# Kernel optimization log

Hardware: AMD Instinct MI355X
Metric: run time of the kernel (lower is better)

Reference implementation:

```python
import jax, jax.numpy as jnp
import numpy as np

NINP = 1024
NHID = 1024
BATCH = 16384
EPS = 1e-5


def _ln(x, g, b):
    mu = jnp.mean(x, axis=-1, keepdims=True)
    var = jnp.mean(jnp.square(x - mu), axis=-1, keepdims=True)
    return (x - mu) * jax.lax.rsqrt(var + EPS) * g + b


def setup_inputs() -> dict:
    key = jax.random.key(0)
    ks = jax.random.split(key, 12)
    s_i = 1.0 / np.sqrt(NINP)
    s_h = 1.0 / np.sqrt(NHID)
    return {
        "inp": jax.random.normal(ks[0], (BATCH, NINP), jnp.float32),
        "hidden": jax.random.normal(ks[1], (BATCH, NHID), jnp.float32),
        "W_i2gate": jax.random.uniform(ks[2], (3 * NHID, NINP), jnp.float32, -s_i, s_i),
        "b_i2gate": jnp.zeros((3 * NHID,), jnp.float32),
        "W_h2gate": jax.random.uniform(ks[3], (3 * NHID, NHID), jnp.float32, -s_h, s_h),
        "b_h2gate": jnp.zeros((3 * NHID,), jnp.float32),
        "W_i2i": jax.random.uniform(ks[4], (NHID, NINP), jnp.float32, -s_i, s_i),
        "b_i2i": jnp.zeros((NHID,), jnp.float32),
        "W_i2h": jax.random.uniform(ks[5], (NHID, NINP), jnp.float32, -s_i, s_i),
        "b_i2h": jnp.zeros((NHID,), jnp.float32),
        "W_h2h": jax.random.uniform(ks[6], (NHID, NHID), jnp.float32, -s_h, s_h),
        "b_h2h": jnp.zeros((NHID,), jnp.float32),
        "g_ig": jnp.ones((3 * NHID,), jnp.float32),
        "be_ig": jnp.zeros((3 * NHID,), jnp.float32),
        "g_hg": jnp.ones((3 * NHID,), jnp.float32),
        "be_hg": jnp.zeros((3 * NHID,), jnp.float32),
        "g_ii": jnp.ones((NHID,), jnp.float32),
        "be_ii": jnp.zeros((NHID,), jnp.float32),
        "g_ih": jnp.ones((NHID,), jnp.float32),
        "be_ih": jnp.zeros((NHID,), jnp.float32),
        "g_hh": jnp.ones((NHID,), jnp.float32),
        "be_hh": jnp.zeros((NHID,), jnp.float32),
    }


def reference(inp, hidden, W_i2gate, b_i2gate, W_h2gate, b_h2gate,
              W_i2i, b_i2i, W_i2h, b_i2h, W_h2h, b_h2h,
              g_ig, be_ig, g_hg, be_hg, g_ii, be_ii,
              g_ih, be_ih, g_hh, be_hh):
    gate = jax.nn.sigmoid(
        _ln(inp @ W_i2gate.T + b_i2gate, g_ig, be_ig)
        + _ln(hidden @ W_h2gate.T + b_h2gate, g_hg, be_hg))
    r, z, g = jnp.split(gate, 3, axis=-1)
    Hx = _ln(inp @ W_i2i.T + b_i2i, g_ii, be_ii)
    xh = _ln(inp @ W_i2h.T + b_i2h, g_ih, be_ih)
    hh = _ln(hidden @ W_h2h.T + b_h2h, g_hh, be_hh)
    hidden_m = jnp.tanh((1.0 - r) * xh + r * hh)
    return ((1.0 - z) * hidden + z * hidden_m) * (1.0 - g) + g * Hx
```

## Files before the change

kernel.cpp:

```cpp
#include <hip/hip_runtime.h>

typedef __bf16 bf16_t;
typedef bf16_t bf16x8 __attribute__((ext_vector_type(8)));
typedef bf16_t bf16x4 __attribute__((ext_vector_type(4)));
typedef float f32x4 __attribute__((ext_vector_type(4)));

#define BATCH 16384
#define KDIM  1024
#define NCOLS 9216

#define BMg 256
#define BNg 256
#define BKg 64
#define NTg (KDIM / BKg)
#define NBN (NCOLS / BNg)

__global__ __launch_bounds__(256)
void cast_all(const float* __restrict__ Wig, const float* __restrict__ Wii,
              const float* __restrict__ Wih, const float* __restrict__ Whg,
              const float* __restrict__ Whh,
              const float* __restrict__ big, const float* __restrict__ bii,
              const float* __restrict__ bih, const float* __restrict__ bhg,
              const float* __restrict__ bhh,
              const float* __restrict__ inp, const float* __restrict__ hid,
              bf16_t* __restrict__ Wcat, float* __restrict__ bcat,
              bf16_t* __restrict__ inpb, bf16_t* __restrict__ hidb,
              int nact_units, int ntot)
{
  int u = blockIdx.x * 256 + threadIdx.x;
  if (u >= ntot) return;

  if (u < 2359296) {
    const float* src; int off;
    if      (u < 786432)  { src = Wig; off = u; }
    else if (u < 1048576) { src = Wii; off = u - 786432; }
    else if (u < 1310720) { src = Wih; off = u - 1048576; }
    else if (u < 2097152) { src = Whg; off = u - 1310720; }
    else                  { src = Whh; off = u - 2097152; }
    float4 v = reinterpret_cast<const float4*>(src)[off];
    bf16x4 o;
    o[0] = (bf16_t)v.x; o[1] = (bf16_t)v.y; o[2] = (bf16_t)v.z; o[3] = (bf16_t)v.w;
    reinterpret_cast<bf16x4*>(Wcat)[u] = o;
  } else if (u < 2361600) {
    int bu = u - 2359296;
    int i = bu * 4;
    const float* src; int off;
    if      (i < 3072) { src = big; off = i; }
    else if (i < 4096) { src = bii; off = i - 3072; }
    else if (i < 5120) { src = bih; off = i - 4096; }
    else if (i < 8192) { src = bhg; off = i - 5120; }
    else               { src = bhh; off = i - 8192; }
    reinterpret_cast<float4*>(bcat)[bu] = *reinterpret_cast<const float4*>(src + off);
  } else {
    int au = u - 2361600;
    const float* src; bf16_t* dst; int off;
    if (au < nact_units) { src = inp; dst = inpb; off = au; }
    else                 { src = hid; dst = hidb; off = au - nact_units; }
    float4 v = reinterpret_cast<const float4*>(src)[off];
    bf16x4 o;
    o[0] = (bf16_t)v.x; o[1] = (bf16_t)v.y; o[2] = (bf16_t)v.z; o[3] = (bf16_t)v.w;
    reinterpret_cast<bf16x4*>(dst)[off] = o;
  }
}

__global__ __launch_bounds__(256)
void cast_acts(const float* __restrict__ inp, const float* __restrict__ hid,
               bf16_t* __restrict__ inpb, bf16_t* __restrict__ hidb, int n4) {
  int i = blockIdx.x * 256 + threadIdx.x;
  if (i >= 2 * n4) return;
  const float* src = (i < n4) ? inp : hid;
  bf16_t* dst = (i < n4) ? inpb : hidb;
  int off = (i < n4) ? i : i - n4;
  float4 v = reinterpret_cast<const float4*>(src)[off];
  bf16x4 o;
  o[0] = (bf16_t)v.x; o[1] = (bf16_t)v.y; o[2] = (bf16_t)v.z; o[3] = (bf16_t)v.w;
  reinterpret_cast<bf16x4*>(dst)[off] = o;
}

__global__ __launch_bounds__(512, 2)
void gemm_preln(const bf16_t* __restrict__ inpb, const bf16_t* __restrict__ hidb,
                const bf16_t* __restrict__ Wcat, const float* __restrict__ bcat,
                bf16_t* __restrict__ preLN, int nbm)
{
  __shared__ alignas(16) char lds_raw[131072];

  const int tid  = threadIdx.x;
  const int wid  = tid >> 6;
  const int lane = tid & 63;
  const int fr   = lane & 15;
  const int kg   = lane >> 4;
  const int wr   = wid >> 2;
  const int wc   = wid & 3;

  const int nwg = nbm * NBN;
  int orig = blockIdx.x;
  int q_ = nwg >> 3, r_ = nwg & 7, xcd = orig & 7, idx = orig >> 3;
  int wg = (xcd < r_ ? xcd * (q_ + 1) : r_ * (q_ + 1) + (xcd - r_) * q_) + idx;
  const int bm = wg / NBN, bn = wg % NBN;
  const int row0 = bm * BMg, col0 = bn * BNg;
  const bf16_t* __restrict__ act = (col0 < 5120) ? inpb : hidb;
  const bf16_t* __restrict__ wgt = Wcat + (size_t)col0 * KDIM;

  const int r_st  = tid >> 2;
  const int k8_st = (tid & 3) ^ ((r_st >> 1) & 3);
  const bf16_t* pA = act + (size_t)(row0 + r_st) * KDIM + k8_st * 8;
  const bf16_t* pB = wgt + (size_t)r_st * KDIM + k8_st * 8;

  auto stage_half = [&](int mat, int h, int T) {
    const bf16_t* s = (mat ? pB : pA) + ((size_t)h * 128) * KDIM + T * BKg;
    char* d = lds_raw + ((T & 1) << 16) + (mat << 15) + (h << 14) + (wid << 10);
    __builtin_amdgcn_global_load_lds(
        (const __attribute__((address_space(1))) unsigned int*)s,
        (__attribute__((address_space(3))) unsigned int*)d, 16, 0, 0);
    __builtin_amdgcn_global_load_lds(
        (const __attribute__((address_space(1))) unsigned int*)(s + 32),
        (__attribute__((address_space(3))) unsigned int*)(d + 8192), 16, 0, 0);
  };

  int offA[4][2], offB[2][2];
  #pragma unroll
  for (int m = 0; m < 4; ++m)
    #pragma unroll
    for (int ks = 0; ks < 2; ++ks) {
      const int rowA = wr * 64 + m * 16 + fr;
      offA[m][ks] = ks * 8192 + rowA * 64 + ((kg ^ ((rowA >> 1) & 3)) << 4);
    }
  #pragma unroll
  for (int n = 0; n < 2; ++n)
    #pragma unroll
    for (int ks = 0; ks < 2; ++ks) {
      const int rowB = wc * 32 + n * 16 + fr;
      offB[n][ks] = ks * 8192 + rowB * 64 + ((kg ^ ((rowB >> 1) & 3)) << 4);
    }

  f32x4 acc[2][4][2][2] = {};

  stage_half(0, 0, 0); stage_half(1, 0, 0);
  stage_half(0, 1, 0); stage_half(1, 1, 0);
  stage_half(0, 0, 1); stage_half(1, 0, 1);
  asm volatile("s_waitcnt vmcnt(4)" ::: "memory");
  __builtin_amdgcn_s_barrier();

  for (int T = 0; T < NTg; ++T) {
    const int bufo = (T & 1) << 16;
    bf16x8 a[4][2], b0[2][2], b1[2][2];

    #pragma unroll
    for (int m = 0; m < 4; ++m)
      #pragma unroll
      for (int ks = 0; ks < 2; ++ks)
        a[m][ks] = *(const bf16x8*)(lds_raw + bufo + offA[m][ks]);
    #pragma unroll
    for (int n = 0; n < 2; ++n)
      #pragma unroll
      for (int ks = 0; ks < 2; ++ks)
        b0[n][ks] = *(const bf16x8*)(lds_raw + bufo + 32768 + offB[n][ks]);
    if (T + 1 < NTg) stage_half(0, 1, T + 1);
    __builtin_amdgcn_s_barrier();
    asm volatile("s_waitcnt lgkmcnt(0)" ::: "memory");
    __builtin_amdgcn_sched_barrier(0);
    __builtin_amdgcn_s_setprio(1);
    #pragma unroll
    for (int m = 0; m < 4; ++m)
      #pragma unroll
      for (int n = 0; n < 2; ++n)
        #pragma unroll
        for (int ks = 0; ks < 2; ++ks)
          acc[0][m][0][n] = __builtin_amdgcn_mfma_f32_16x16x32_bf16(a[m][ks], b0[n][ks], acc[0][m][0][n], 0, 0, 0);
    __builtin_amdgcn_s_setprio(0);
    __builtin_amdgcn_s_barrier();

    #pragma unroll
    for (int n = 0; n < 2; ++n)
      #pragma unroll
      for (int ks = 0; ks < 2; ++ks)
        b1[n][ks] = *(const bf16x8*)(lds_raw + bufo + 32768 + 16384 + offB[n][ks]);
    if (T + 1 < NTg) stage_half(1, 1, T + 1);
    __builtin_amdgcn_s_barrier();
    asm volatile("s_waitcnt lgkmcnt(0)" ::: "memory");
    __builtin_amdgcn_sched_barrier(0);
    __builtin_amdgcn_s_setprio(1);
    #pragma unroll
    for (int m = 0; m < 4; ++m)
      #pragma unroll
      for (int n = 0; n < 2; ++n)
        #pragma unroll
        for (int ks = 0; ks < 2; ++ks)
          acc[0][m][1][n] = __builtin_amdgcn_mfma_f32_16x16x32_bf16(a[m][ks], b1[n][ks], acc[0][m][1][n], 0, 0, 0);
    __builtin_amdgcn_s_setprio(0);
    __builtin_amdgcn_s_barrier();

    #pragma unroll
    for (int m = 0; m < 4; ++m)
      #pragma unroll
      for (int ks = 0; ks < 2; ++ks)
        a[m][ks] = *(const bf16x8*)(lds_raw + bufo + 16384 + offA[m][ks]);
    if (T + 2 < NTg) stage_half(0, 0, T + 2);
    __builtin_amdgcn_s_barrier();
    asm volatile("s_waitcnt lgkmcnt(0)" ::: "memory");
    __builtin_amdgcn_sched_barrier(0);
    __builtin_amdgcn_s_setprio(1);
    #pragma unroll
    for (int m = 0; m < 4; ++m)
      #pragma unroll
      for (int n = 0; n < 2; ++n)
        #pragma unroll
        for (int ks = 0; ks < 2; ++ks)
          acc[1][m][1][n] = __builtin_amdgcn_mfma_f32_16x16x32_bf16(a[m][ks], b1[n][ks], acc[1][m][1][n], 0, 0, 0);
    __builtin_amdgcn_s_setprio(0);
    __builtin_amdgcn_s_barrier();

    if (T + 2 < NTg) stage_half(1, 0, T + 2);
    __builtin_amdgcn_s_barrier();
    __builtin_amdgcn_s_setprio(1);
    #pragma unroll
    for (int m = 0; m < 4; ++m)
      #pragma unroll
      for (int n = 0; n < 2; ++n)
        #pragma unroll
        for (int ks = 0; ks < 2; ++ks)
          acc[1][m][0][n] = __builtin_amdgcn_mfma_f32_16x16x32_bf16(a[m][ks], b0[n][ks], acc[1][m][0][n], 0, 0, 0);
    __builtin_amdgcn_s_setprio(0);

    if (T < NTg - 2) {
      asm volatile("s_waitcnt vmcnt(4)" ::: "memory");
      __builtin_amdgcn_s_barrier();
    } else if (T == NTg - 2) {
      asm volatile("s_waitcnt vmcnt(0)" ::: "memory");
      __builtin_amdgcn_s_barrier();
    }
  }

  #pragma unroll
  for (int qn_ = 0; qn_ < 2; ++qn_)
    #pragma unroll
    for (int n = 0; n < 2; ++n) {
      const int col = col0 + qn_ * 128 + wc * 32 + n * 16 + fr;
      const float bias = bcat[col];
      #pragma unroll
      for (int qm_ = 0; qm_ < 2; ++qm_)
        #pragma unroll
        for (int m = 0; m < 4; ++m) {
          const int rbase = row0 + qm_ * 128 + wr * 64 + m * 16 + kg * 4;
          #pragma unroll
          for (int j = 0; j < 4; ++j)
            preLN[(size_t)(rbase + j) * NCOLS + col] = (bf16_t)(acc[qm_][m][qn_][n][j] + bias);
        }
    }
}

__global__ __launch_bounds__(256)
void ln_combine(const bf16_t* __restrict__ preLN, const float* __restrict__ hidden,
                const float* __restrict__ g_ig, const float* __restrict__ be_ig,
                const float* __restrict__ g_hg, const float* __restrict__ be_hg,
                const float* __restrict__ g_ii, const float* __restrict__ be_ii,
                const float* __restrict__ g_ih, const float* __restrict__ be_ih,
                const float* __restrict__ g_hh, const float* __restrict__ be_hh,
                float* __restrict__ out)
{
  __shared__ alignas(16) bf16_t rowbuf[NCOLS];
  __shared__ float wsum[4][10];
  __shared__ float stats[10];
  const int tid = threadIdx.x;
  const int wv  = tid >> 6;
  const int ln  = tid & 63;
  const size_t row = blockIdx.x;
  const bf16_t* __restrict__ src = preLN + row * NCOLS;

  float s1[5] = {0.f, 0.f, 0.f, 0.f, 0.f};
  float s2[5] = {0.f, 0.f, 0.f, 0.f, 0.f};
  #pragma unroll
  for (int j = 0; j < 9; ++j) {
    const int idx = j * 1024 + tid * 4;
    bf16x4 v = *(const bf16x4*)&src[idx];
    *(bf16x4*)&rowbuf[idx] = v;
    const int sg = (j < 3) ? 0 : (j == 3) ? 1 : (j == 4) ? 2 : (j < 8) ? 3 : 4;
    const float f0 = (float)v[0], f1 = (float)v[1], f2 = (float)v[2], f3 = (float)v[3];
    s1[sg] += f0 + f1 + f2 + f3;
    s2[sg] += f0 * f0 + f1 * f1 + f2 * f2 + f3 * f3;
  }
  #pragma unroll
  for (int s = 0; s < 5; ++s)
    #pragma unroll
    for (int off = 32; off; off >>= 1) {
      s1[s] += __shfl_xor(s1[s], off);
      s2[s] += __shfl_xor(s2[s], off);
    }
  if (ln == 0) {
    #pragma unroll
    for (int s = 0; s < 5; ++s) { wsum[wv][s] = s1[s]; wsum[wv][5 + s] = s2[s]; }
  }
  __syncthreads();
  if (tid < 5) {
    const float n = (tid == 0 || tid == 3) ? 3072.f : 1024.f;
    float t1 = wsum[0][tid] + wsum[1][tid] + wsum[2][tid] + wsum[3][tid];
    float t2 = wsum[0][5 + tid] + wsum[1][5 + tid] + wsum[2][5 + tid] + wsum[3][5 + tid];
    float mu = t1 / n;
    float var = t2 / n - mu * mu;
    stats[tid] = mu;
    stats[5 + tid] = rsqrtf(var + 1e-5f);
  }
  __syncthreads();

  const float mu0 = stats[0], r0 = stats[5];
  const float mu1 = stats[1], r1 = stats[6];
  const float mu2 = stats[2], r2 = stats[7];
  const float mu3 = stats[3], r3 = stats[8];
  const float mu4 = stats[4], r4 = stats[9];
  const float* __restrict__ hrow = hidden + row * 1024;

  const int c = tid * 4;
  bf16x4 v_igr = *(const bf16x4*)&rowbuf[c];
  bf16x4 v_igz = *(const bf16x4*)&rowbuf[c + 1024];
  bf16x4 v_igg = *(const bf16x4*)&rowbuf[c + 2048];
  bf16x4 v_ii  = *(const bf16x4*)&rowbuf[c + 3072];
  bf16x4 v_ih  = *(const bf16x4*)&rowbuf[c + 4096];
  bf16x4 v_hgr = *(const bf16x4*)&rowbuf[c + 5120];
  bf16x4 v_hgz = *(const bf16x4*)&rowbuf[c + 6144];
  bf16x4 v_hgg = *(const bf16x4*)&rowbuf[c + 7168];
  bf16x4 v_hh  = *(const bf16x4*)&rowbuf[c + 8192];

  f32x4 Gr  = *(const f32x4*)&g_ig[c];        f32x4 Br  = *(const f32x4*)&be_ig[c];
  f32x4 Gz  = *(const f32x4*)&g_ig[c + 1024]; f32x4 Bz  = *(const f32x4*)&be_ig[c + 1024];
  f32x4 Gg  = *(const f32x4*)&g_ig[c + 2048]; f32x4 Bg  = *(const f32x4*)&be_ig[c + 2048];
  f32x4 Hr  = *(const f32x4*)&g_hg[c];        f32x4 Cr  = *(const f32x4*)&be_hg[c];
  f32x4 Hz  = *(const f32x4*)&g_hg[c + 1024]; f32x4 Cz  = *(const f32x4*)&be_hg[c + 1024];
  f32x4 Hg  = *(const f32x4*)&g_hg[c + 2048]; f32x4 Cg  = *(const f32x4*)&be_hg[c + 2048];
  f32x4 Gii = *(const f32x4*)&g_ii[c];        f32x4 Bii = *(const f32x4*)&be_ii[c];
  f32x4 Gih = *(const f32x4*)&g_ih[c];        f32x4 Bih = *(const f32x4*)&be_ih[c];
  f32x4 Ghh = *(const f32x4*)&g_hh[c];        f32x4 Bhh = *(const f32x4*)&be_hh[c];
  f32x4 hv  = *(const f32x4*)&hrow[c];

  f32x4 o;
  #pragma unroll
  for (int i = 0; i < 4; ++i) {
    float pr = ((float)v_igr[i] - mu0) * r0 * Gr[i] + Br[i]
             + ((float)v_hgr[i] - mu3) * r3 * Hr[i] + Cr[i];
    float pz = ((float)v_igz[i] - mu0) * r0 * Gz[i] + Bz[i]
             + ((float)v_hgz[i] - mu3) * r3 * Hz[i] + Cz[i];
    float pg = ((float)v_igg[i] - mu0) * r0 * Gg[i] + Bg[i]
             + ((float)v_hgg[i] - mu3) * r3 * Hg[i] + Cg[i];

    float rr = 1.f / (1.f + __expf(-pr));
    float zz = 1.f / (1.f + __expf(-pz));
    float gg = 1.f / (1.f + __expf(-pg));

    float Hx = ((float)v_ii[i] - mu1) * r1 * Gii[i] + Bii[i];
    float xh = ((float)v_ih[i] - mu2) * r2 * Gih[i] + Bih[i];
    float hh = ((float)v_hh[i] - mu4) * r4 * Ghh[i] + Bhh[i];

    float pre = (1.f - rr) * xh + rr * hh;
    float hm  = 1.f - 2.f / (1.f + __expf(2.f * pre));
    o[i] = ((1.f - zz) * hv[i] + zz * hm) * (1.f - gg) + gg * Hx;
  }
  *(f32x4*)&out[row * 1024 + c] = o;
}

extern "C" void kernel_launch(void* const* d_in, const int* in_sizes, int n_in,
                              void* d_out, int out_size, void* d_ws, size_t ws_size,
                              hipStream_t stream) {
  const float* inp      = (const float*)d_in[0];
  const float* hidden   = (const float*)d_in[1];
  const float* W_i2gate = (const float*)d_in[2];
  const float* b_i2gate = (const float*)d_in[3];
  const float* W_h2gate = (const float*)d_in[4];
  const float* b_h2gate = (const float*)d_in[5];
  const float* W_i2i    = (const float*)d_in[6];
  const float* b_i2i    = (const float*)d_in[7];
  const float* W_i2h    = (const float*)d_in[8];
  const float* b_i2h    = (const float*)d_in[9];
  const float* W_h2h    = (const float*)d_in[10];
  const float* b_h2h    = (const float*)d_in[11];
  const float* g_ig  = (const float*)d_in[12];
  const float* be_ig = (const float*)d_in[13];
  const float* g_hg  = (const float*)d_in[14];
  const float* be_hg = (const float*)d_in[15];
  const float* g_ii  = (const float*)d_in[16];
  const float* be_ii = (const float*)d_in[17];
  const float* g_ih  = (const float*)d_in[18];
  const float* be_ih = (const float*)d_in[19];
  const float* g_hh  = (const float*)d_in[20];
  const float* be_hh = (const float*)d_in[21];
  float* out = (float*)d_out;

  const size_t WCAT_B  = (size_t)NCOLS * KDIM * 2;
  const size_t BCAT_B  = (size_t)NCOLS * 4;
  const size_t FIXED_B = WCAT_B + BCAT_B;
  const size_t PER_ROW = 2048 + 2048 + 18432;

  if (ws_size < FIXED_B + PER_ROW * 256) return;

  char* ws = (char*)d_ws;
  bf16_t* Wcat = (bf16_t*)ws;
  float*  bcat = (float*)(ws + WCAT_B);
  char*   dyn  = ws + FIXED_B;

  size_t max_rows = (ws_size - FIXED_B) / PER_ROW;
  int chunk = (int)((max_rows / 256) * 256);
  if (chunk > BATCH) chunk = BATCH;

  bf16_t* inpb  = (bf16_t*)dyn;
  bf16_t* hidb  = (bf16_t*)(dyn + (size_t)chunk * 2048);
  bf16_t* preLN = (bf16_t*)(dyn + (size_t)chunk * 4096);

  if (chunk == BATCH) {
    const int nact = BATCH * KDIM / 4;
    const int ntot = 2361600 + 2 * nact;
    cast_all<<<(ntot + 255) / 256, 256, 0, stream>>>(
        W_i2gate, W_i2i, W_i2h, W_h2gate, W_h2h,
        b_i2gate, b_i2i, b_i2h, b_h2gate, b_h2h,
        inp, hidden, Wcat, bcat, inpb, hidb, nact, ntot);

    int nbm = BATCH / BMg;
    gemm_preln<<<nbm * NBN, 512, 0, stream>>>(inpb, hidb, Wcat, bcat, preLN, nbm);

    ln_combine<<<BATCH, 256, 0, stream>>>(preLN, hidden,
                                          g_ig, be_ig, g_hg, be_hg,
                                          g_ii, be_ii, g_ih, be_ih, g_hh, be_hh,
                                          out);
  } else {
    const int ntot_w = 2361600;
    cast_all<<<(ntot_w + 255) / 256, 256, 0, stream>>>(
        W_i2gate, W_i2i, W_i2h, W_h2gate, W_h2h,
        b_i2gate, b_i2i, b_i2h, b_h2gate, b_h2h,
        nullptr, nullptr, Wcat, bcat, nullptr, nullptr, 0, ntot_w);

    for (int r0 = 0; r0 < BATCH; r0 += chunk) {
      int cr = BATCH - r0;
      if (cr > chunk) cr = chunk;
      int n4 = cr * KDIM / 4;
      cast_acts<<<(2 * n4 + 255) / 256, 256, 0, stream>>>(
          inp + (size_t)r0 * KDIM, hidden + (size_t)r0 * KDIM, inpb, hidb, n4);

      int nbm = cr / BMg;
      gemm_preln<<<nbm * NBN, 512, 0, stream>>>(inpb, hidb, Wcat, bcat, preLN, nbm);

      ln_combine<<<cr, 256, 0, stream>>>(preLN, hidden + (size_t)r0 * KDIM,
                                         g_ig, be_ig, g_hg, be_hg,
                                         g_ii, be_ii, g_ih, be_ih, g_hh, be_hh,
                                         out + (size_t)r0 * KDIM);
    }
  }
}
```

Measured before the change: 499.7 us.

## Switch GEMM to 32x32x16 MFMA and process multiple rows per LN block

The GEMM inner loops move from 16x16x32 bf16 MFMA tiles to 32x32x16 tiles, which changes the LDS fragment offsets, the accumulator layout and the epilogue row mapping. This cuts the number of MFMA issues and LDS reads per tile. Separately, the LayerNorm/combine kernel now handles 8 rows per block, loading gamma/beta once per block and prefetching the next row's preLN values while reducing the current row. The cost is more complex accumulator indexing, and each LN block runs longer in exchange for less per-row setup.

```diff
diff --git a/kernel.cpp b/kernel.cpp
--- a/kernel.cpp
+++ b/kernel.cpp
@@ -4,6 +4,7 @@
 typedef bf16_t bf16x8 __attribute__((ext_vector_type(8)));
 typedef bf16_t bf16x4 __attribute__((ext_vector_type(4)));
 typedef float f32x4 __attribute__((ext_vector_type(4)));
+typedef float f32x16 __attribute__((ext_vector_type(16)));
 
 #define BATCH 16384
 #define KDIM  1024
@@ -14,6 +15,7 @@
 #define BKg 64
 #define NTg (KDIM / BKg)
 #define NBN (NCOLS / BNg)
+#define LNROWS 8
 
 __global__ __launch_bounds__(256)
 void cast_all(const float* __restrict__ Wig, const float* __restrict__ Wii,
@@ -87,8 +89,8 @@
   const int tid  = threadIdx.x;
   const int wid  = tid >> 6;
   const int lane = tid & 63;
-  const int fr   = lane & 15;
-  const int kg   = lane >> 4;
+  const int l31  = lane & 31;
+  const int lk   = lane >> 5;
   const int wr   = wid >> 2;
   const int wc   = wid & 3;
 
@@ -117,23 +119,23 @@
         (__attribute__((address_space(3))) unsigned int*)(d + 8192), 16, 0, 0);
   };
 
-  int offA[4][2], offB[2][2];
+  int offA[2][4], offB[4];
   #pragma unroll
-  for (int m = 0; m < 4; ++m)
-    #pragma unroll
-    for (int ks = 0; ks < 2; ++ks) {
-      const int rowA = wr * 64 + m * 16 + fr;
-      offA[m][ks] = ks * 8192 + rowA * 64 + ((kg ^ ((rowA >> 1) & 3)) << 4);
+  for (int t = 0; t < 2; ++t)
+    #pragma unroll
+    for (int ks = 0; ks < 4; ++ks) {
+      const int rowA = wr * 64 + t * 32 + l31;
+      const int k8 = (ks & 1) * 2 + lk;
+      offA[t][ks] = (ks >> 1) * 8192 + rowA * 64 + ((k8 ^ ((rowA >> 1) & 3)) << 4);
     }
   #pragma unroll
-  for (int n = 0; n < 2; ++n)
-    #pragma unroll
-    for (int ks = 0; ks < 2; ++ks) {
-      const int rowB = wc * 32 + n * 16 + fr;
-      offB[n][ks] = ks * 8192 + rowB * 64 + ((kg ^ ((rowB >> 1) & 3)) << 4);
-    }
-
-  f32x4 acc[2][4][2][2] = {};
+  for (int ks = 0; ks < 4; ++ks) {
+    const int colB = wc * 32 + l31;
+    const int k8 = (ks & 1) * 2 + lk;
+    offB[ks] = (ks >> 1) * 8192 + colB * 64 + ((k8 ^ ((colB >> 1) & 3)) << 4);
+  }
+
+  f32x16 acc[2][2][2] = {};
 
   stage_half(0, 0, 0); stage_half(1, 0, 0);
   stage_half(0, 1, 0); stage_half(1, 1, 0);
@@ -143,70 +145,60 @@
 
   for (int T = 0; T < NTg; ++T) {
     const int bufo = (T & 1) << 16;
-    bf16x8 a[4][2], b0[2][2], b1[2][2];
-
-    #pragma unroll
-    for (int m = 0; m < 4; ++m)
-      #pragma unroll
-      for (int ks = 0; ks < 2; ++ks)
-        a[m][ks] = *(const bf16x8*)(lds_raw + bufo + offA[m][ks]);
-    #pragma unroll
-    for (int n = 0; n < 2; ++n)
-      #pragma unroll
-      for (int ks = 0; ks < 2; ++ks)
-        b0[n][ks] = *(const bf16x8*)(lds_raw + bufo + 32768 + offB[n][ks]);
+    bf16x8 a[2][4], b0[4], b1[4];
+
+    #pragma unroll
+    for (int t = 0; t < 2; ++t)
+      #pragma unroll
+      for (int ks = 0; ks < 4; ++ks)
+        a[t][ks] = *(const bf16x8*)(lds_raw + bufo + offA[t][ks]);
+    #pragma unroll
+    for (int ks = 0; ks < 4; ++ks)
+      b0[ks] = *(const bf16x8*)(lds_raw + bufo + 32768 + offB[ks]);
     if (T + 1 < NTg) stage_half(0, 1, T + 1);
     __builtin_amdgcn_s_barrier();
     asm volatile("s_waitcnt lgkmcnt(0)" ::: "memory");
     __builtin_amdgcn_sched_barrier(0);
     __builtin_amdgcn_s_setprio(1);
     #pragma unroll
-    for (int m = 0; m < 4; ++m)
-      #pragma unroll
-      for (int n = 0; n < 2; ++n)
-        #pragma unroll
-        for (int ks = 0; ks < 2; ++ks)
-          acc[0][m][0][n] = __builtin_amdgcn_mfma_f32_16x16x32_bf16(a[m][ks], b0[n][ks], acc[0][m][0][n], 0, 0, 0);
+    for (int t = 0; t < 2; ++t)
+      #pragma unroll
+      for (int ks = 0; ks < 4; ++ks)
+        acc[0][t][0] = __builtin_amdgcn_mfma_f32_32x32x16_bf16(a[t][ks], b0[ks], acc[0][t][0], 0, 0, 0);
     __builtin_amdgcn_s_setprio(0);
     __builtin_amdgcn_s_barrier();
 
     #pragma unroll
-    for (int n = 0; n < 2; ++n)
-      #pragma unroll
-      for (int ks = 0; ks < 2; ++ks)
-        b1[n][ks] = *(const bf16x8*)(lds_raw + bufo + 32768 + 16384 + offB[n][ks]);
+    for (int ks = 0; ks < 4; ++ks)
+      b1[ks] = *(const bf16x8*)(lds_raw + bufo + 32768 + 16384 + offB[ks]);
     if (T + 1 < NTg) stage_half(1, 1, T + 1);
     __builtin_amdgcn_s_barrier();
     asm volatile("s_waitcnt lgkmcnt(0)" ::: "memory");
     __builtin_amdgcn_sched_barrier(0);
     __builtin_amdgcn_s_setprio(1);
     #pragma unroll
-    for (int m = 0; m < 4; ++m)
-      #pragma unroll
-      for (int n = 0; n < 2; ++n)
-        #pragma unroll
-        for (int ks = 0; ks < 2; ++ks)
-          acc[0][m][1][n] = __builtin_amdgcn_mfma_f32_16x16x32_bf16(a[m][ks], b1[n][ks], acc[0][m][1][n], 0, 0, 0);
+    for (int t = 0; t < 2; ++t)
+      #pragma unroll
+      for (int ks = 0; ks < 4; ++ks)
+        acc[0][t][1] = __builtin_amdgcn_mfma_f32_32x32x16_bf16(a[t][ks], b1[ks], acc[0][t][1], 0, 0, 0);
     __builtin_amdgcn_s_setprio(0);
     __builtin_amdgcn_s_barrier();
 
     #pragma unroll
-    for (int m = 0; m < 4; ++m)
-      #pragma unroll
-      for (int ks = 0; ks < 2; ++ks)
-        a[m][ks] = *(const bf16x8*)(lds_raw + bufo + 16384 + offA[m][ks]);
+    for (int t = 0; t < 2; ++t)
+      #pragma unroll
+      for (int ks = 0; ks < 4; ++ks)
+        a[t][ks] = *(const bf16x8*)(lds_raw + bufo + 16384 + offA[t][ks]);
     if (T + 2 < NTg) stage_half(0, 0, T + 2);
     __builtin_amdgcn_s_barrier();
     asm volatile("s_waitcnt lgkmcnt(0)" ::: "memory");
     __builtin_amdgcn_sched_barrier(0);
     __builtin_amdgcn_s_setprio(1);
     #pragma unroll
-    for (int m = 0; m < 4; ++m)
-      #pragma unroll
-      for (int n = 0; n < 2; ++n)
-        #pragma unroll
-        for (int ks = 0; ks < 2; ++ks)
-          acc[1][m][1][n] = __builtin_amdgcn_mfma_f32_16x16x32_bf16(a[m][ks], b1[n][ks], acc[1][m][1][n], 0, 0, 0);
+    for (int t = 0; t < 2; ++t)
+      #pragma unroll
+      for (int ks = 0; ks < 4; ++ks)
+        acc[1][t][1] = __builtin_amdgcn_mfma_f32_32x32x16_bf16(a[t][ks], b1[ks], acc[1][t][1], 0, 0, 0);
     __builtin_amdgcn_s_setprio(0);
     __builtin_amdgcn_s_barrier();
 
@@ -214,12 +206,10 @@
     __builtin_amdgcn_s_barrier();
     __builtin_amdgcn_s_setprio(1);
     #pragma unroll
-    for (int m = 0; m < 4; ++m)
-      #pragma unroll
-      for (int n = 0; n < 2; ++n)
-        #pragma unroll
-        for (int ks = 0; ks < 2; ++ks)
-          acc[1][m][0][n] = __builtin_amdgcn_mfma_f32_16x16x32_bf16(a[m][ks], b0[n][ks], acc[1][m][0][n], 0, 0, 0);
+    for (int t = 0; t < 2; ++t)
+      #pragma unroll
+      for (int ks = 0; ks < 4; ++ks)
+        acc[1][t][0] = __builtin_amdgcn_mfma_f32_32x32x16_bf16(a[t][ks], b0[ks], acc[1][t][0], 0, 0, 0);
     __builtin_amdgcn_s_setprio(0);
 
     if (T < NTg - 2) {
@@ -232,21 +222,21 @@
   }
 
   #pragma unroll
-  for (int qn_ = 0; qn_ < 2; ++qn_)
-    #pragma unroll
-    for (int n = 0; n < 2; ++n) {
-      const int col = col0 + qn_ * 128 + wc * 32 + n * 16 + fr;
-      const float bias = bcat[col];
-      #pragma unroll
-      for (int qm_ = 0; qm_ < 2; ++qm_)
+  for (int qn_ = 0; qn_ < 2; ++qn_) {
+    const int col = col0 + qn_ * 128 + wc * 32 + l31;
+    const float bias = bcat[col];
+    #pragma unroll
+    for (int qm_ = 0; qm_ < 2; ++qm_)
+      #pragma unroll
+      for (int t = 0; t < 2; ++t) {
+        const int rbase = row0 + qm_ * 128 + wr * 64 + t * 32 + 4 * lk;
         #pragma unroll
-        for (int m = 0; m < 4; ++m) {
-          const int rbase = row0 + qm_ * 128 + wr * 64 + m * 16 + kg * 4;
-          #pragma unroll
-          for (int j = 0; j < 4; ++j)
-            preLN[(size_t)(rbase + j) * NCOLS + col] = (bf16_t)(acc[qm_][m][qn_][n][j] + bias);
+        for (int reg = 0; reg < 16; ++reg) {
+          const int rr = rbase + (reg & 3) + 8 * (reg >> 2);
+          preLN[(size_t)rr * NCOLS + col] = (bf16_t)(acc[qm_][t][qn_][reg] + bias);
         }
-    }
+      }
+  }
 }
 
 __global__ __launch_bounds__(256)
@@ -264,96 +254,116 @@
   const int tid = threadIdx.x;
   const int wv  = tid >> 6;
   const int ln  = tid & 63;
-  const size_t row = blockIdx.x;
-  const bf16_t* __restrict__ src = preLN + row * NCOLS;
-
-  float s1[5] = {0.f, 0.f, 0.f, 0.f, 0.f};
-  float s2[5] = {0.f, 0.f, 0.f, 0.f, 0.f};
-  #pragma unroll
-  for (int j = 0; j < 9; ++j) {
-    const int idx = j * 1024 + tid * 4;
-    bf16x4 v = *(const bf16x4*)&src[idx];
-    *(bf16x4*)&rowbuf[idx] = v;
-    const int sg = (j < 3) ? 0 : (j == 3) ? 1 : (j == 4) ? 2 : (j < 8) ? 3 : 4;
-    const float f0 = (float)v[0], f1 = (float)v[1], f2 = (float)v[2], f3 = (float)v[3];
-    s1[sg] += f0 + f1 + f2 + f3;
-    s2[sg] += f0 * f0 + f1 * f1 + f2 * f2 + f3 * f3;
-  }
-  #pragma unroll
-  for (int s = 0; s < 5; ++s)
-    #pragma unroll
-    for (int off = 32; off; off >>= 1) {
-      s1[s] += __shfl_xor(s1[s], off);
-      s2[s] += __shfl_xor(s2[s], off);
-    }
-  if (ln == 0) {
-    #pragma unroll
-    for (int s = 0; s < 5; ++s) { wsum[wv][s] = s1[s]; wsum[wv][5 + s] = s2[s]; }
-  }
-  __syncthreads();
-  if (tid < 5) {
-    const float n = (tid == 0 || tid == 3) ? 3072.f : 1024.f;
-    float t1 = wsum[0][tid] + wsum[1][tid] + wsum[2][tid] + wsum[3][tid];
-    float t2 = wsum[0][5 + tid] + wsum[1][5 + tid] + wsum[2][5 + tid] + wsum[3][5 + tid];
-    float mu = t1 / n;
-    float var = t2 / n - mu * mu;
-    stats[tid] = mu;
-    stats[5 + tid] = rsqrtf(var + 1e-5f);
-  }
-  __syncthreads();
-
-  const float mu0 = stats[0], r0 = stats[5];
-  const float mu1 = stats[1], r1 = stats[6];
-  const float mu2 = stats[2], r2 = stats[7];
-  const float mu3 = stats[3], r3 = stats[8];
-  const float mu4 = stats[4], r4 = stats[9];
-  const float* __restrict__ hrow = hidden + row * 1024;
+  const size_t row0 = (size_t)blockIdx.x * LNROWS;
 
   const int c = tid * 4;
-  bf16x4 v_igr = *(const bf16x4*)&rowbuf[c];
-  bf16x4 v_igz = *(const bf16x4*)&rowbuf[c + 1024];
-  bf16x4 v_igg = *(const bf16x4*)&rowbuf[c + 2048];
-  bf16x4 v_ii  = *(const bf16x4*)&rowbuf[c + 3072];
-  bf16x4 v_ih  = *(const bf16x4*)&rowbuf[c + 4096];
-  bf16x4 v_hgr = *(const bf16x4*)&rowbuf[c + 5120];
-  bf16x4 v_hgz = *(const bf16x4*)&rowbuf[c + 6144];
-  bf16x4 v_hgg = *(const bf16x4*)&rowbuf[c + 7168];
-  bf16x4 v_hh  = *(const bf16x4*)&rowbuf[c + 8192];
-
-  f32x4 Gr  = *(const f32x4*)&g_ig[c];        f32x4 Br  = *(const f32x4*)&be_ig[c];
-  f32x4 Gz  = *(const f32x4*)&g_ig[c + 1024]; f32x4 Bz  = *(const f32x4*)&be_ig[c + 1024];
-  f32x4 Gg  = *(const f32x4*)&g_ig[c + 2048]; f32x4 Bg  = *(const f32x4*)&be_ig[c + 2048];
-  f32x4 Hr  = *(const f32x4*)&g_hg[c];        f32x4 Cr  = *(const f32x4*)&be_hg[c];
-  f32x4 Hz  = *(const f32x4*)&g_hg[c + 1024]; f32x4 Cz  = *(const f32x4*)&be_hg[c + 1024];
-  f32x4 Hg  = *(const f32x4*)&g_hg[c + 2048]; f32x4 Cg  = *(const f32x4*)&be_hg[c + 2048];
-  f32x4 Gii = *(const f32x4*)&g_ii[c];        f32x4 Bii = *(const f32x4*)&be_ii[c];
-  f32x4 Gih = *(const f32x4*)&g_ih[c];        f32x4 Bih = *(const f32x4*)&be_ih[c];
-  f32x4 Ghh = *(const f32x4*)&g_hh[c];        f32x4 Bhh = *(const f32x4*)&be_hh[c];
-  f32x4 hv  = *(const f32x4*)&hrow[c];
-
-  f32x4 o;
-  #pragma unroll
-  for (int i = 0; i < 4; ++i) {
-    float pr = ((float)v_igr[i] - mu0) * r0 * Gr[i] + Br[i]
-             + ((float)v_hgr[i] - mu3) * r3 * Hr[i] + Cr[i];
-    float pz = ((float)v_igz[i] - mu0) * r0 * Gz[i] + Bz[i]
-             + ((float)v_hgz[i] - mu3) * r3 * Hz[i] + Cz[i];
-    float pg = ((float)v_igg[i] - mu0) * r0 * Gg[i] + Bg[i]
-             + ((float)v_hgg[i] - mu3) * r3 * Hg[i] + Cg[i];
-
-    float rr = 1.f / (1.f + __expf(-pr));
-    float zz = 1.f / (1.f + __expf(-pz));
-    float gg = 1.f / (1.f + __expf(-pg));
-
-    float Hx = ((float)v_ii[i] - mu1) * r1 * Gii[i] + Bii[i];
-    float xh = ((float)v_ih[i] - mu2) * r2 * Gih[i] + Bih[i];
-    float hh = ((float)v_hh[i] - mu4) * r4 * Ghh[i] + Bhh[i];
-
-    float pre = (1.f - rr) * xh + rr * hh;
-    float hm  = 1.f - 2.f / (1.f + __expf(2.f * pre));
-    o[i] = ((1.f - zz) * hv[i] + zz * hm) * (1.f - gg) + gg * Hx;
-  }
-  *(f32x4*)&out[row * 1024 + c] = o;
+  const f32x4 Gr  = *(const f32x4*)&g_ig[c];        const f32x4 Br  = *(const f32x4*)&be_ig[c];
+  const f32x4 Gz  = *(const f32x4*)&g_ig[c + 1024]; const f32x4 Bz  = *(const f32x4*)&be_ig[c + 1024];
+  const f32x4 Gg  = *(const f32x4*)&g_ig[c + 2048]; const f32x4 Bg  = *(const f32x4*)&be_ig[c + 2048];
+  const f32x4 Hr  = *(const f32x4*)&g_hg[c];        const f32x4 Cr  = *(const f32x4*)&be_hg[c];
+  const f32x4 Hz  = *(const f32x4*)&g_hg[c + 1024]; const f32x4 Cz  = *(const f32x4*)&be_hg[c + 1024];
+  const f32x4 Hg  = *(const f32x4*)&g_hg[c + 2048]; const f32x4 Cg  = *(const f32x4*)&be_hg[c + 2048];
+  const f32x4 Gii = *(const f32x4*)&g_ii[c];        const f32x4 Bii = *(const f32x4*)&be_ii[c];
+  const f32x4 Gih = *(const f32x4*)&g_ih[c];        const f32x4 Bih = *(const f32x4*)&be_ih[c];
+  const f32x4 Ghh = *(const f32x4*)&g_hh[c];        const f32x4 Bhh = *(const f32x4*)&be_hh[c];
+
+  bf16x4 v[9];
+  {
+    const bf16_t* src = preLN + row0 * NCOLS;
+    #pragma unroll
+    for (int j = 0; j < 9; ++j)
+      v[j] = *(const bf16x4*)&src[j * 1024 + c];
+  }
+
+  for (int r = 0; r < LNROWS; ++r) {
+    const size_t row = row0 + r;
+
+    float s1[5] = {0.f, 0.f, 0.f, 0.f, 0.f};
+    float s2[5] = {0.f, 0.f, 0.f, 0.f, 0.f};
+    #pragma unroll
+    for (int j = 0; j < 9; ++j) {
+      *(bf16x4*)&rowbuf[j * 1024 + c] = v[j];
+      const int sg = (j < 3) ? 0 : (j == 3) ? 1 : (j == 4) ? 2 : (j < 8) ? 3 : 4;
+      const float f0 = (float)v[j][0], f1 = (float)v[j][1], f2 = (float)v[j][2], f3 = (float)v[j][3];
+      s1[sg] += f0 + f1 + f2 + f3;
+      s2[sg] += f0 * f0 + f1 * f1 + f2 * f2 + f3 * f3;
+    }
+
+    if (r + 1 < LNROWS) {
+      const bf16_t* nsrc = preLN + (row + 1) * NCOLS;
+      #pragma unroll
+      for (int j = 0; j < 9; ++j)
+        v[j] = *(const bf16x4*)&nsrc[j * 1024 + c];
+    }
+
+    #pragma unroll
+    for (int s = 0; s < 5; ++s)
+      #pragma unroll
+      for (int off = 32; off; off >>= 1) {
+        s1[s] += __shfl_xor(s1[s], off);
+        s2[s] += __shfl_xor(s2[s], off);
+      }
+    if (ln == 0) {
+      #pragma unroll
+      for (int s = 0; s < 5; ++s) { wsum[wv][s] = s1[s]; wsum[wv][5 + s] = s2[s]; }
+    }
+    asm volatile("s_waitcnt lgkmcnt(0)" ::: "memory");
+    __builtin_amdgcn_s_barrier();
+    if (tid < 5) {
+      const float n = (tid == 0 || tid == 3) ? 3072.f : 1024.f;
+      float t1 = wsum[0][tid] + wsum[1][tid] + wsum[2][tid] + wsum[3][tid];
+      float t2 = wsum[0][5 + tid] + wsum[1][5 + tid] + wsum[2][5 + tid] + wsum[3][5 + tid];
+      float mu = t1 / n;
+      stats[tid] = mu;
+      stats[5 + tid] = rsqrtf(t2 / n - mu * mu + 1e-5f);
+    }
+    asm volatile("s_waitcnt lgkmcnt(0)" ::: "memory");
+    __builtin_amdgcn_s_barrier();
+
+    const float mu0 = stats[0], r0s = stats[5];
+    const float mu1 = stats[1], r1s = stats[6];
+    const float mu2 = stats[2], r2s = stats[7];
+    const float mu3 = stats[3], r3s = stats[8];
+    const float mu4 = stats[4], r4s = stats[9];
+
+    bf16x4 v_igr = *(const bf16x4*)&rowbuf[c];
+    bf16x4 v_igz = *(const bf16x4*)&rowbuf[c + 1024];
+    bf16x4 v_igg = *(const bf16x4*)&rowbuf[c + 2048];
+    bf16x4 v_ii  = *(const bf16x4*)&rowbuf[c + 3072];
+    bf16x4 v_ih  = *(const bf16x4*)&rowbuf[c + 4096];
+    bf16x4 v_hgr = *(const bf16x4*)&rowbuf[c + 5120];
+    bf16x4 v_hgz = *(const bf16x4*)&rowbuf[c + 6144];
+    bf16x4 v_hgg = *(const bf16x4*)&rowbuf[c + 7168];
+    bf16x4 v_hh  = *(const bf16x4*)&rowbuf[c + 8192];
+    f32x4 hv = *(const f32x4*)&hidden[row * 1024 + c];
+
+    f32x4 o;
+    #pragma unroll
+    for (int i = 0; i < 4; ++i) {
+      float pr = ((float)v_igr[i] - mu0) * r0s * Gr[i] + Br[i]
+               + ((float)v_hgr[i] - mu3) * r3s * Hr[i] + Cr[i];
+      float pz = ((float)v_igz[i] - mu0) * r0s * Gz[i] + Bz[i]
+               + ((float)v_hgz[i] - mu3) * r3s * Hz[i] + Cz[i];
+      float pg = ((float)v_igg[i] - mu0) * r0s * Gg[i] + Bg[i]
+               + ((float)v_hgg[i] - mu3) * r3s * Hg[i] + Cg[i];
+
+      float rr = 1.f / (1.f + __expf(-pr));
+      float zz = 1.f / (1.f + __expf(-pz));
+      float gg = 1.f / (1.f + __expf(-pg));
+
+      float Hx = ((float)v_ii[i] - mu1) * r1s * Gii[i] + Bii[i];
+      float xh = ((float)v_ih[i] - mu2) * r2s * Gih[i] + Bih[i];
+      float hh = ((float)v_hh[i] - mu4) * r4s * Ghh[i] + Bhh[i];
+
+      float pre = (1.f - rr) * xh + rr * hh;
+      float hm  = 1.f - 2.f / (1.f + __expf(2.f * pre));
+      o[i] = ((1.f - zz) * hv[i] + zz * hm) * (1.f - gg) + gg * Hx;
+    }
+    *(f32x4*)&out[row * 1024 + c] = o;
+
+    asm volatile("s_waitcnt lgkmcnt(0)" ::: "memory");
+    __builtin_amdgcn_s_barrier();
+  }
 }
 
 extern "C" void kernel_launch(void* const* d_in, const int* in_sizes, int n_in,
@@ -414,7 +424,7 @@
     int nbm = BATCH / BMg;
     gemm_preln<<<nbm * NBN, 512, 0, stream>>>(inpb, hidb, Wcat, bcat, preLN, nbm);
 
-    ln_combine<<<BATCH, 256, 0, stream>>>(preLN, hidden,
+    ln_combine<<<BATCH / LNROWS, 256, 0, stream>>>(preLN, hidden,
                                           g_ig, be_ig, g_hg, be_hg,
                                           g_ii, be_ii, g_ih, be_ih, g_hh, be_hh,
                                           out);
@@ -435,7 +445,7 @@
       int nbm = cr / BMg;
       gemm_preln<<<nbm * NBN, 512, 0, stream>>>(inpb, hidb, Wcat, bcat, preLN, nbm);
 
-      ln_combine<<<cr, 256, 0, stream>>>(preLN, hidden + (size_t)r0 * KDIM,
+      ln_combine<<<cr / LNROWS, 256, 0, stream>>>(preLN, hidden + (size_t)r0 * KDIM,
                                          g_ig, be_ig, g_hg, be_hg,
                                          g_ii, be_ii, g_ih, be_ih, g_hh, be_hh,
                                          out + (size_t)r0 * KDIM);
```

Result: slower. 538.6 us (+7.8%).

## Merge GEMM main-loop phases from four to two and widen LN row loads

Applied to the files above, without the earlier changes.

The GEMM inner loop is restructured from four MFMA phases, each with its own barriers and LDS reads, into two phases. The first loads both B halves and issues both next-tile stage_halfs; the second reloads A and issues both T+2 stages. This cuts barrier count and exposes larger MFMA batches, at the cost of more live registers and less interleaving of global loads with compute. The LN combine kernel also switches from bf16x4 to bf16x8 loads in fewer iterations, using per-half-block segment mapping for the row statistics.

```diff
diff --git a/kernel.cpp b/kernel.cpp
--- a/kernel.cpp
+++ b/kernel.cpp
@@ -153,9 +153,11 @@
     #pragma unroll
     for (int n = 0; n < 2; ++n)
       #pragma unroll
-      for (int ks = 0; ks < 2; ++ks)
+      for (int ks = 0; ks < 2; ++ks) {
         b0[n][ks] = *(const bf16x8*)(lds_raw + bufo + 32768 + offB[n][ks]);
-    if (T + 1 < NTg) stage_half(0, 1, T + 1);
+        b1[n][ks] = *(const bf16x8*)(lds_raw + bufo + 32768 + 16384 + offB[n][ks]);
+      }
+    if (T + 1 < NTg) { stage_half(0, 1, T + 1); stage_half(1, 1, T + 1); }
     __builtin_amdgcn_s_barrier();
     asm volatile("s_waitcnt lgkmcnt(0)" ::: "memory");
     __builtin_amdgcn_sched_barrier(0);
@@ -163,19 +165,22 @@
     #pragma unroll
     for (int m = 0; m < 4; ++m)
       #pragma unroll
-      for (int n = 0; n < 2; ++n)
+      for (int ks = 0; ks < 2; ++ks) {
         #pragma unroll
-        for (int ks = 0; ks < 2; ++ks)
+        for (int n = 0; n < 2; ++n) {
           acc[0][m][0][n] = __builtin_amdgcn_mfma_f32_16x16x32_bf16(a[m][ks], b0[n][ks], acc[0][m][0][n], 0, 0, 0);
+          acc[0][m][1][n] = __builtin_amdgcn_mfma_f32_16x16x32_bf16(a[m][ks], b1[n][ks], acc[0][m][1][n], 0, 0, 0);
+        }
+      }
     __builtin_amdgcn_s_setprio(0);
     __builtin_amdgcn_s_barrier();
 
     #pragma unroll
-    for (int n = 0; n < 2; ++n)
+    for (int m = 0; m < 4; ++m)
       #pragma unroll
       for (int ks = 0; ks < 2; ++ks)
-        b1[n][ks] = *(const bf16x8*)(lds_raw + bufo + 32768 + 16384 + offB[n][ks]);
-    if (T + 1 < NTg) stage_half(1, 1, T + 1);
+        a[m][ks] = *(const bf16x8*)(lds_raw + bufo + 16384 + offA[m][ks]);
+    if (T + 2 < NTg) { stage_half(0, 0, T + 2); stage_half(1, 0, T + 2); }
     __builtin_amdgcn_s_barrier();
     asm volatile("s_waitcnt lgkmcnt(0)" ::: "memory");
     __builtin_amdgcn_sched_barrier(0);
@@ -183,43 +188,13 @@
     #pragma unroll
     for (int m = 0; m < 4; ++m)
       #pragma unroll
-      for (int n = 0; n < 2; ++n)
+      for (int ks = 0; ks < 2; ++ks) {
         #pragma unroll
-        for (int ks = 0; ks < 2; ++ks)
-          acc[0][m][1][n] = __builtin_amdgcn_mfma_f32_16x16x32_bf16(a[m][ks], b1[n][ks], acc[0][m][1][n], 0, 0, 0);
-    __builtin_amdgcn_s_setprio(0);
-    __builtin_amdgcn_s_barrier();
-
-    #pragma unroll
-    for (int m = 0; m < 4; ++m)
-      #pragma unroll
-      for (int ks = 0; ks < 2; ++ks)
-        a[m][ks] = *(const bf16x8*)(lds_raw + bufo + 16384 + offA[m][ks]);
-    if (T + 2 < NTg) stage_half(0, 0, T + 2);
-    __builtin_amdgcn_s_barrier();
-    asm volatile("s_waitcnt lgkmcnt(0)" ::: "memory");
-    __builtin_amdgcn_sched_barrier(0);
-    __builtin_amdgcn_s_setprio(1);
-    #pragma unroll
-    for (int m = 0; m < 4; ++m)
-      #pragma unroll
-      for (int n = 0; n < 2; ++n)
-        #pragma unroll
-        for (int ks = 0; ks < 2; ++ks)
+        for (int n = 0; n < 2; ++n) {
+          acc[1][m][0][n] = __builtin_amdgcn_mfma_f32_16x16x32_bf16(a[m][ks], b0[n][ks], acc[1][m][0][n], 0, 0, 0);
           acc[1][m][1][n] = __builtin_amdgcn_mfma_f32_16x16x32_bf16(a[m][ks], b1[n][ks], acc[1][m][1][n], 0, 0, 0);
-    __builtin_amdgcn_s_setprio(0);
-    __builtin_amdgcn_s_barrier();
-
-    if (T + 2 < NTg) stage_half(1, 0, T + 2);
-    __builtin_amdgcn_s_barrier();
-    __builtin_amdgcn_s_setprio(1);
-    #pragma unroll
-    for (int m = 0; m < 4; ++m)
-      #pragma unroll
-      for (int n = 0; n < 2; ++n)
-        #pragma unroll
-        for (int ks = 0; ks < 2; ++ks)
-          acc[1][m][0][n] = __builtin_amdgcn_mfma_f32_16x16x32_bf16(a[m][ks], b0[n][ks], acc[1][m][0][n], 0, 0, 0);
+        }
+      }
     __builtin_amdgcn_s_setprio(0);
 
     if (T < NTg - 2) {
@@ -264,21 +239,33 @@
   const int tid = threadIdx.x;
   const int wv  = tid >> 6;
   const int ln  = tid & 63;
+  const int hi  = tid >> 7;
   const size_t row = blockIdx.x;
   const bf16_t* __restrict__ src = preLN + row * NCOLS;
 
   float s1[5] = {0.f, 0.f, 0.f, 0.f, 0.f};
   float s2[5] = {0.f, 0.f, 0.f, 0.f, 0.f};
   #pragma unroll
-  for (int j = 0; j < 9; ++j) {
-    const int idx = j * 1024 + tid * 4;
-    bf16x4 v = *(const bf16x4*)&src[idx];
-    *(bf16x4*)&rowbuf[idx] = v;
-    const int sg = (j < 3) ? 0 : (j == 3) ? 1 : (j == 4) ? 2 : (j < 8) ? 3 : 4;
-    const float f0 = (float)v[0], f1 = (float)v[1], f2 = (float)v[2], f3 = (float)v[3];
-    s1[sg] += f0 + f1 + f2 + f3;
-    s2[sg] += f0 * f0 + f1 * f1 + f2 * f2 + f3 * f3;
-  }
+  for (int j = 0; j < 4; ++j) {
+    const int idx = j * 2048 + tid * 8;
+    bf16x8 v = *(const bf16x8*)&src[idx];
+    *(bf16x8*)&rowbuf[idx] = v;
+    float fs = 0.f, fq = 0.f;
+    #pragma unroll
+    for (int t = 0; t < 8; ++t) { float f = (float)v[t]; fs += f; fq += f * f; }
+    constexpr int kSG0[4] = {0, 0, 2, 3};
+    constexpr int kSG1[4] = {0, 1, 3, 3};
+    if (hi == 0) { s1[kSG0[j]] += fs; s2[kSG0[j]] += fq; }
+    else         { s1[kSG1[j]] += fs; s2[kSG1[j]] += fq; }
+  }
+  if (hi == 0) {
+    const int idx = 8192 + tid * 8;
+    bf16x8 v = *(const bf16x8*)&src[idx];
+    *(bf16x8*)&rowbuf[idx] = v;
+    #pragma unroll
+    for (int t = 0; t < 8; ++t) { float f = (float)v[t]; s1[4] += f; s2[4] += f * f; }
+  }
+
   #pragma unroll
   for (int s = 0; s < 5; ++s)
     #pragma unroll
```

Measured after the change: 506.9 us. About the same (+1.4%).
